# Performance work log

Measured on AMD Instinct MI355X. Metric: run time of the kernel, lower is better.

## Reference

```python
import jax, jax.numpy as jnp
import numpy as np

NUM_HEADS = 8
HEAD_DIM = 16  # d_model=128 / 8 heads
SCALE = HEAD_DIM ** -0.5


def setup_inputs() -> dict:
    key = jax.random.key(0)
    ks = jax.random.split(key, 12)
    B, A, K, L, D, M = 8, 64, 16, 30, 128, 128
    s = 1.0 / np.sqrt(D)
    inp = {
        "future_feat": jax.random.normal(ks[0], (B, A, L, D), jnp.float32),
        "geom_bias": jax.random.normal(ks[1], (B, A, K), jnp.float32),
        "Wq": jax.random.normal(ks[2], (D, M), jnp.float32) * s,
        "bq": jnp.zeros((M,), jnp.float32),
        "Wk": jax.random.normal(ks[3], (D, M), jnp.float32) * s,
        "bk": jnp.zeros((M,), jnp.float32),
        "Wv": jax.random.normal(ks[4], (D, M), jnp.float32) * s,
        "bv": jnp.zeros((M,), jnp.float32),
        "Wo": jax.random.normal(ks[5], (M, M), jnp.float32) * s,
        "bo": jnp.zeros((M,), jnp.float32),
        "neighbour_indices": jax.random.randint(ks[6], (B, A, K), 0, A),
        "neighbour_mask": jax.random.randint(ks[7], (B, A, K), 0, 2).astype(bool),
    }
    return inp


def reference(future_feat, geom_bias, Wq, bq, Wk, bk, Wv, bv, Wo, bo,
              neighbour_indices, neighbour_mask):
    B, A, L, D = future_feat.shape
    K = neighbour_indices.shape[2]
    H, HD = NUM_HEADS, HEAD_DIM

    # gather neighbour futures: [B, A, K, L, D]
    neighbours = jax.vmap(lambda f, idx: f[idx])(future_feat, neighbour_indices)

    q = (future_feat @ Wq + bq).reshape(B, A, L, H, HD).transpose(0, 1, 3, 2, 4)      # [B,A,H,Lq,hd]
    k = (neighbours @ Wk + bk).reshape(B, A, K, L, H, HD).transpose(0, 1, 4, 2, 3, 5)  # [B,A,H,K,Lk,hd]
    v = (neighbours @ Wv + bv).reshape(B, A, K, L, H, HD).transpose(0, 1, 4, 2, 3, 5)  # [B,A,H,K,Lk,hd]

    scores = jnp.einsum('bahqd,bahkld->bahqkl', q, k) * SCALE                          # [B,A,H,Lq,K,Lk]
    scores = scores + geom_bias[:, :, None, None, :, None]
    scores = jnp.where(neighbour_mask[:, :, None, None, :, None], scores, -jnp.inf)

    attn = jax.nn.softmax(scores.reshape(B, A, H, L, K * L), axis=-1)
    attn = jnp.nan_to_num(attn).reshape(B, A, H, L, K, L)

    ctx = jnp.einsum('bahqkl,bahkld->bahqd', attn, v)                                  # [B,A,H,Lq,hd]
    ctx = ctx.transpose(0, 1, 3, 2, 4).reshape(B, A, L, H * HD)
    out = ctx @ Wo + bo                                                                # [B,A,Lq,d_model]
    return out, attn
```

## Files before the change

kernel.cpp:

```cpp
#include <hip/hip_runtime.h>
#include <math.h>


#define NB 8
#define NA 64
#define NK 16
#define NL 30
#define ND 128
#define NM 128
#define NH 8
#define NHD 16
#define NKK (NK*NL)
#define FSCALE 0.25f
#define NROWS (NB*NA*NL)

typedef __attribute__((ext_vector_type(8))) short bf16x8;
typedef __attribute__((ext_vector_type(4))) float f32x4;

__device__ __forceinline__ unsigned short bf16r(float x) {
    unsigned u = __float_as_uint(x);
    return (unsigned short)((u + 0x7fffu + ((u >> 16) & 1u)) >> 16);
}

__global__ void detect_mask_fmt(const unsigned int* __restrict__ m, int* __restrict__ flag)
{
    __shared__ int not_i32, not_f32;
    if (threadIdx.x == 0) { not_i32 = 0; not_f32 = 0; }
    __syncthreads();
    for (int i = threadIdx.x; i < 2048; i += 256) {
        unsigned int u = m[i];
        if (u > 1u) not_i32 = 1;
        if (u != 0u && u != 0x3F800000u) not_f32 = 1;
    }
    __syncthreads();
    if (threadIdx.x == 0) *flag = (!not_i32) ? 0 : ((!not_f32) ? 1 : 2);
}

__global__ __launch_bounds__(256) void proj_qkv(
    const float* __restrict__ x,
    const float* __restrict__ Wq, const float* __restrict__ bq,
    const float* __restrict__ Wk, const float* __restrict__ bk,
    const float* __restrict__ Wv, const float* __restrict__ bv,
    float* __restrict__ qp, float* __restrict__ kp, float* __restrict__ vp)
{
    __shared__ __align__(16) float xs[NL][ND];
    const int ba = blockIdx.x;
    const float* xrow = x + (size_t)ba * NL * ND;
    for (int i = threadIdx.x; i < NL*ND/4; i += 256)
        ((float4*)xs)[i] = ((const float4*)xrow)[i];
    __syncthreads();

    const int j  = threadIdx.x & 127;
    const int rh = threadIdx.x >> 7;
    const float* Ws[3] = {Wq, Wk, Wv};
    const float* bs[3] = {bq, bk, bv};
    float*       Os[3] = {qp, kp, vp};

    #pragma unroll
    for (int m = 0; m < 3; ++m) {
        const float* W = Ws[m];
        float acc[15];
        #pragma unroll
        for (int r = 0; r < 15; ++r) acc[r] = 0.f;
        for (int d = 0; d < ND; d += 4) {
            float w0 = W[(d+0)*NM + j];
            float w1 = W[(d+1)*NM + j];
            float w2 = W[(d+2)*NM + j];
            float w3 = W[(d+3)*NM + j];
            #pragma unroll
            for (int r = 0; r < 15; ++r) {
                float4 xv = *(const float4*)&xs[rh*15 + r][d];
                acc[r] = fmaf(xv.x, w0, acc[r]);
                acc[r] = fmaf(xv.y, w1, acc[r]);
                acc[r] = fmaf(xv.z, w2, acc[r]);
                acc[r] = fmaf(xv.w, w3, acc[r]);
            }
        }
        float bj = bs[m][j];
        float* O = Os[m] + ((size_t)ba*NL + rh*15)*NM + j;
        #pragma unroll
        for (int r = 0; r < 15; ++r) O[r*NM] = acc[r] + bj;
    }
}

__global__ __launch_bounds__(128, 2) void attn_kernel(
    const float* __restrict__ qp, const float* __restrict__ kp, const float* __restrict__ vp,
    const float* __restrict__ geom_bias, const int* __restrict__ nidx,
    const void* __restrict__ nmask, const int* __restrict__ mask_fmt,
    float* __restrict__ attn_out, float* __restrict__ ctx_out)
{
    __shared__ __align__(16) short Kbf[NKK][16];
    __shared__ __align__(16) short Vt[16][488];
    __shared__ __align__(16) short pbuf[2][16][40];
    __shared__ float bias_ext[NKK];
    __shared__ float biasm[NK];
    __shared__ int   idx_s[NK];

    const int t    = threadIdx.x;
    const int blk  = blockIdx.x;
    const int h    = blk & 7;
    const int ba   = blk >> 3;
    const int b    = ba >> 6;
    const int lane = t & 63;
    const int w    = t >> 6;
    const int n    = lane & 15;
    const int quad = lane >> 4;

    if (t < NK) {
        idx_s[t] = nidx[ba*NK + t];
        const int fmt = *mask_fmt;
        bool mv;
        if (fmt == 0)      mv = ((const int*)nmask)[ba*NK + t] != 0;
        else if (fmt == 1) mv = ((const float*)nmask)[ba*NK + t] != 0.0f;
        else               mv = ((const unsigned char*)nmask)[ba*NK + t] != 0;
        biasm[t] = mv ? geom_bias[ba*NK + t] : -INFINITY;
    }
    __syncthreads();

    for (int i = t; i < NKK*4; i += 128) {
        const int kk = i >> 2, p = i & 3;
        const int kn = kk / NL, l = kk - kn*NL;
        const size_t off = ((size_t)(b*NA + idx_s[kn])*NL + l)*NM + h*NHD + p*4;
        float4 kv = *(const float4*)(kp + off);
        unsigned long long pk =
              (unsigned long long)bf16r(kv.x)
            | ((unsigned long long)bf16r(kv.y) << 16)
            | ((unsigned long long)bf16r(kv.z) << 32)
            | ((unsigned long long)bf16r(kv.w) << 48);
        *(unsigned long long*)&Kbf[kk][p*4] = pk;
        float4 vv = *(const float4*)(vp + off);
        Vt[p*4+0][kk] = (short)bf16r(vv.x);
        Vt[p*4+1][kk] = (short)bf16r(vv.y);
        Vt[p*4+2][kk] = (short)bf16r(vv.z);
        Vt[p*4+3][kk] = (short)bf16r(vv.w);
    }
    for (int i = t; i < NKK; i += 128) bias_ext[i] = biasm[i / NL];

    bf16x8 a_hi, a_lo;
    #pragma unroll
    for (int j = 0; j < 8; ++j) { a_hi[j] = 0; a_lo[j] = 0; }
    const int qrow = w*16 + n;
    if (quad < 2 && qrow < NL) {
        const float* qb = qp + ((size_t)ba*NL + qrow)*NM + h*NHD + quad*8;
        float4 x0 = *(const float4*)(qb);
        float4 x1 = *(const float4*)(qb + 4);
        float xv[8] = {x0.x,x0.y,x0.z,x0.w,x1.x,x1.y,x1.z,x1.w};
        #pragma unroll
        for (int j = 0; j < 8; ++j) {
            float x = xv[j] * FSCALE;
            unsigned short hb = bf16r(x);
            a_hi[j] = (short)hb;
            a_lo[j] = (short)bf16r(x - __uint_as_float(((unsigned)hb) << 16));
        }
    }
    __syncthreads();

    float s[NL][4];
    #pragma unroll
    for (int tt = 0; tt < NL; ++tt) {
        bf16x8 bfrag;
        #pragma unroll
        for (int j = 0; j < 8; ++j) bfrag[j] = 0;
        if (quad < 2)
            bfrag = *(const bf16x8*)&Kbf[tt*16 + n][quad*8];
        f32x4 acc = {0.f, 0.f, 0.f, 0.f};
        acc = __builtin_amdgcn_mfma_f32_16x16x32_bf16(a_hi, bfrag, acc, 0, 0, 0);
        acc = __builtin_amdgcn_mfma_f32_16x16x32_bf16(a_lo, bfrag, acc, 0, 0, 0);
        const float bv = bias_ext[tt*16 + n];
        s[tt][0] = acc[0] + bv;
        s[tt][1] = acc[1] + bv;
        s[tt][2] = acc[2] + bv;
        s[tt][3] = acc[3] + bv;
    }

    #pragma unroll
    for (int r = 0; r < 4; ++r) {
        float m = -INFINITY;
        #pragma unroll
        for (int tt = 0; tt < NL; ++tt) m = fmaxf(m, s[tt][r]);
        m = fmaxf(m, __shfl_xor(m, 1));
        m = fmaxf(m, __shfl_xor(m, 2));
        m = fmaxf(m, __shfl_xor(m, 4));
        m = fmaxf(m, __shfl_xor(m, 8));
        const bool ok = (m > -INFINITY);
        float sum = 0.f;
        #pragma unroll
        for (int tt = 0; tt < NL; ++tt) {
            float p = ok ? __expf(s[tt][r] - m) : 0.f;
            s[tt][r] = p;
            sum += p;
        }
        sum += __shfl_xor(sum, 1);
        sum += __shfl_xor(sum, 2);
        sum += __shfl_xor(sum, 4);
        sum += __shfl_xor(sum, 8);
        const float inv = (sum > 0.f) ? 1.f / sum : 0.f;
        #pragma unroll
        for (int tt = 0; tt < NL; ++tt) s[tt][r] *= inv;
    }

    const size_t abase = (size_t)blk * NL * NKK;
    #pragma unroll
    for (int r = 0; r < 4; ++r) {
        const int qr = w*16 + quad*4 + r;
        if (qr < NL) {
            float* ap = attn_out + abase + (size_t)qr * NKK + n;
            #pragma unroll
            for (int tt = 0; tt < NL; ++tt) ap[tt*16] = s[tt][r];
        }
    }

    f32x4 ctx = {0.f, 0.f, 0.f, 0.f};
    #pragma unroll
    for (int c = 0; c < 15; ++c) {
        #pragma unroll
        for (int r = 0; r < 4; ++r) {
            pbuf[w][quad*4 + r][n]      = (short)bf16r(s[2*c    ][r]);
            pbuf[w][quad*4 + r][16 + n] = (short)bf16r(s[2*c + 1][r]);
        }
        bf16x8 pa = *(const bf16x8*)&pbuf[w][n][quad*8];
        bf16x8 vb = *(const bf16x8*)&Vt[n][c*32 + quad*8];
        ctx = __builtin_amdgcn_mfma_f32_16x16x32_bf16(pa, vb, ctx, 0, 0, 0);
    }

    #pragma unroll
    for (int r = 0; r < 4; ++r) {
        const int qr = w*16 + quad*4 + r;
        if (qr < NL)
            ctx_out[((size_t)ba*NL + qr)*NM + h*NHD + n] = ctx[r];
    }
}

__global__ __launch_bounds__(256) void out_proj(
    const float* __restrict__ ctx, const float* __restrict__ Wo,
    const float* __restrict__ bo, float* __restrict__ out)
{
    __shared__ __align__(16) float xs[NL][ND];
    const int ba = blockIdx.x;
    const float* xrow = ctx + (size_t)ba * NL * ND;
    for (int i = threadIdx.x; i < NL*ND/4; i += 256)
        ((float4*)xs)[i] = ((const float4*)xrow)[i];
    __syncthreads();

    const int j  = threadIdx.x & 127;
    const int rh = threadIdx.x >> 7;
    float acc[15];
    #pragma unroll
    for (int r = 0; r < 15; ++r) acc[r] = 0.f;
    for (int d = 0; d < ND; d += 4) {
        float w0 = Wo[(d+0)*NM + j];
        float w1 = Wo[(d+1)*NM + j];
        float w2 = Wo[(d+2)*NM + j];
        float w3 = Wo[(d+3)*NM + j];
        #pragma unroll
        for (int r = 0; r < 15; ++r) {
            float4 xv = *(const float4*)&xs[rh*15 + r][d];
            acc[r] = fmaf(xv.x, w0, acc[r]);
            acc[r] = fmaf(xv.y, w1, acc[r]);
            acc[r] = fmaf(xv.z, w2, acc[r]);
            acc[r] = fmaf(xv.w, w3, acc[r]);
        }
    }
    float bj = bo[j];
    float* O = out + ((size_t)ba*NL + rh*15)*NM + j;
    #pragma unroll
    for (int r = 0; r < 15; ++r) O[r*NM] = acc[r] + bj;
}

extern "C" void kernel_launch(void* const* d_in, const int* in_sizes, int n_in,
                              void* d_out, int out_size, void* d_ws, size_t ws_size,
                              hipStream_t stream)
{
    const float* x    = (const float*)d_in[0];
    const float* gb   = (const float*)d_in[1];
    const float* Wq   = (const float*)d_in[2];
    const float* bq   = (const float*)d_in[3];
    const float* Wk   = (const float*)d_in[4];
    const float* bk   = (const float*)d_in[5];
    const float* Wv   = (const float*)d_in[6];
    const float* bv   = (const float*)d_in[7];
    const float* Wo   = (const float*)d_in[8];
    const float* bo   = (const float*)d_in[9];
    const int*   nidx = (const int*)d_in[10];
    const void*  nmask= d_in[11];

    float* out  = (float*)d_out;
    float* attn = out + (size_t)NROWS * NM;

    float* qp = (float*)d_ws;
    float* kp = qp + (size_t)NROWS * NM;
    float* vp = kp + (size_t)NROWS * NM;
    int* mflag = (int*)(vp + (size_t)NROWS * NM);

    detect_mask_fmt<<<1, 256, 0, stream>>>((const unsigned int*)nmask, mflag);
    proj_qkv<<<NB*NA, 256, 0, stream>>>(x, Wq, bq, Wk, bk, Wv, bv, qp, kp, vp);
    attn_kernel<<<NB*NA*NH, 128, 0, stream>>>(qp, kp, vp, gb, nidx, nmask, mflag,
                                              attn,  out);
    out_proj<<<NB*NA, 256, 0, stream>>>(out, Wo, bo, out);
}
```

Measured before the change: 389.6 us.

## Move Q/K/V and output projections to split-bf16 MFMA and coalesce attn stores

Replaces the scalar FP32 projection kernels with an MFMA kernel that uses hi/lo bf16 splits of activations and pre-transposed weights. A prep kernel converts the weights into this format and also folds in mask-format detection and bias staging. The attention kernel now stages probabilities in shared memory so that attn rows are written with contiguous float4 stores instead of strided scalar ones. The split-bf16 scheme (3 MFMAs) only approximates FP32 precision, and the extra shared-memory staging adds LDS traffic.

```diff
diff --git a/kernel.cpp b/kernel.cpp
--- a/kernel.cpp
+++ b/kernel.cpp
@@ -21,65 +21,122 @@
     unsigned u = __float_as_uint(x);
     return (unsigned short)((u + 0x7fffu + ((u >> 16) & 1u)) >> 16);
 }
-
-__global__ void detect_mask_fmt(const unsigned int* __restrict__ m, int* __restrict__ flag)
+__device__ __forceinline__ float bf16tof(unsigned short h) {
+    return __uint_as_float((unsigned)h << 16);
+}
+
+__global__ __launch_bounds__(256) void prep_kernel(
+    const float* __restrict__ Wq, const float* __restrict__ Wk,
+    const float* __restrict__ Wv, const float* __restrict__ Wo,
+    const float* __restrict__ bq, const float* __restrict__ bk,
+    const float* __restrict__ bv, const float* __restrict__ bo,
+    const unsigned int* __restrict__ nmask_u, int* __restrict__ mflag,
+    short* __restrict__ WtH, short* __restrict__ WtL, float* __restrict__ bias_ws)
 {
-    __shared__ int not_i32, not_f32;
-    if (threadIdx.x == 0) { not_i32 = 0; not_f32 = 0; }
+    const int t = threadIdx.x;
+    if (blockIdx.x == 8) {
+        __shared__ int not_i32, not_f32;
+        if (t == 0) { not_i32 = 0; not_f32 = 0; }
+        __syncthreads();
+        for (int i = t; i < 2048; i += 256) {
+            unsigned u = nmask_u[i];
+            if (u > 1u) not_i32 = 1;
+            if (u != 0u && u != 0x3F800000u) not_f32 = 1;
+        }
+        __syncthreads();
+        if (t == 0) *mflag = (!not_i32) ? 0 : ((!not_f32) ? 1 : 2);
+        if (t < 128) {
+            bias_ws[t]       = bq[t];
+            bias_ws[128 + t] = bk[t];
+            bias_ws[256 + t] = bv[t];
+            bias_ws[384 + t] = bo[t];
+        }
+        return;
+    }
+    const int m = blockIdx.x >> 1, half = blockIdx.x & 1, d0 = half * 64;
+    const float* W = (m == 0) ? Wq : (m == 1) ? Wk : (m == 2) ? Wv : Wo;
+    __shared__ __align__(16) float xs[64][132];
+    for (int i = t; i < 2048; i += 256) {
+        const int dd = i >> 5, j4 = (i & 31) * 4;
+        *(float4*)&xs[dd][j4] = *(const float4*)(W + (size_t)(d0 + dd) * NM + j4);
+    }
     __syncthreads();
-    for (int i = threadIdx.x; i < 2048; i += 256) {
-        unsigned int u = m[i];
-        if (u > 1u) not_i32 = 1;
-        if (u != 0u && u != 0x3F800000u) not_f32 = 1;
-    }
-    __syncthreads();
-    if (threadIdx.x == 0) *flag = (!not_i32) ? 0 : ((!not_f32) ? 1 : 2);
-}
-
-__global__ __launch_bounds__(256) void proj_qkv(
-    const float* __restrict__ x,
-    const float* __restrict__ Wq, const float* __restrict__ bq,
-    const float* __restrict__ Wk, const float* __restrict__ bk,
-    const float* __restrict__ Wv, const float* __restrict__ bv,
-    float* __restrict__ qp, float* __restrict__ kp, float* __restrict__ vp)
+    const int n = t >> 1, hs = t & 1;
+    unsigned short hb[32], lb[32];
+    #pragma unroll
+    for (int s = 0; s < 32; ++s) {
+        float v = xs[hs*32 + s][n];
+        unsigned short h = bf16r(v);
+        hb[s] = h;
+        lb[s] = bf16r(v - bf16tof(h));
+    }
+    const size_t base = (size_t)m * 16384 + (size_t)n * 128 + d0 + hs * 32;
+    #pragma unroll
+    for (int g = 0; g < 8; ++g) {
+        unsigned long long ph =
+              (unsigned long long)hb[4*g]
+            | ((unsigned long long)hb[4*g+1] << 16)
+            | ((unsigned long long)hb[4*g+2] << 32)
+            | ((unsigned long long)hb[4*g+3] << 48);
+        unsigned long long pl =
+              (unsigned long long)lb[4*g]
+            | ((unsigned long long)lb[4*g+1] << 16)
+            | ((unsigned long long)lb[4*g+2] << 32)
+            | ((unsigned long long)lb[4*g+3] << 48);
+        *(unsigned long long*)(WtH + base + g*4) = ph;
+        *(unsigned long long*)(WtL + base + g*4) = pl;
+    }
+}
+
+__global__ __launch_bounds__(256) void proj_mfma(
+    const float* X,
+    const short* __restrict__ WtH, const short* __restrict__ WtL,
+    const float* __restrict__ bias_ws,
+    float* Y, int mat_off)
 {
-    __shared__ __align__(16) float xs[NL][ND];
-    const int ba = blockIdx.x;
-    const float* xrow = x + (size_t)ba * NL * ND;
-    for (int i = threadIdx.x; i < NL*ND/4; i += 256)
-        ((float4*)xs)[i] = ((const float4*)xrow)[i];
-    __syncthreads();
-
-    const int j  = threadIdx.x & 127;
-    const int rh = threadIdx.x >> 7;
-    const float* Ws[3] = {Wq, Wk, Wv};
-    const float* bs[3] = {bq, bk, bv};
-    float*       Os[3] = {qp, kp, vp};
-
-    #pragma unroll
-    for (int m = 0; m < 3; ++m) {
-        const float* W = Ws[m];
-        float acc[15];
-        #pragma unroll
-        for (int r = 0; r < 15; ++r) acc[r] = 0.f;
-        for (int d = 0; d < ND; d += 4) {
-            float w0 = W[(d+0)*NM + j];
-            float w1 = W[(d+1)*NM + j];
-            float w2 = W[(d+2)*NM + j];
-            float w3 = W[(d+3)*NM + j];
-            #pragma unroll
-            for (int r = 0; r < 15; ++r) {
-                float4 xv = *(const float4*)&xs[rh*15 + r][d];
-                acc[r] = fmaf(xv.x, w0, acc[r]);
-                acc[r] = fmaf(xv.y, w1, acc[r]);
-                acc[r] = fmaf(xv.z, w2, acc[r]);
-                acc[r] = fmaf(xv.w, w3, acc[r]);
-            }
-        }
-        float bj = bs[m][j];
-        float* O = Os[m] + ((size_t)ba*NL + rh*15)*NM + j;
-        #pragma unroll
-        for (int r = 0; r < 15; ++r) O[r*NM] = acc[r] + bj;
+    const int m    = blockIdx.y;
+    const int mi   = mat_off + m;
+    const int rt   = blockIdx.x;
+    const int t    = threadIdx.x;
+    const int lane = t & 63, w = t >> 6;
+    const int n    = lane & 15, quad = lane >> 4;
+
+    const short* wh = WtH + (size_t)mi * 16384;
+    const short* wl = WtL + (size_t)mi * 16384;
+
+    const int arow = rt*64 + w*16 + n;
+    const float* xr = X + (size_t)arow * ND;
+    bf16x8 Ah[4], Al[4];
+    #pragma unroll
+    for (int ks = 0; ks < 4; ++ks) {
+        float4 x0 = *(const float4*)(xr + ks*32 + quad*8);
+        float4 x1 = *(const float4*)(xr + ks*32 + quad*8 + 4);
+        float xv[8] = {x0.x,x0.y,x0.z,x0.w,x1.x,x1.y,x1.z,x1.w};
+        #pragma unroll
+        for (int j = 0; j < 8; ++j) {
+            unsigned short h = bf16r(xv[j]);
+            Ah[ks][j] = (short)h;
+            Al[ks][j] = (short)bf16r(xv[j] - bf16tof(h));
+        }
+    }
+
+    float* ym = Y + (size_t)m * NROWS * NM;
+    #pragma unroll
+    for (int nt = 0; nt < 8; ++nt) {
+        f32x4 acc = {0.f, 0.f, 0.f, 0.f};
+        #pragma unroll
+        for (int ks = 0; ks < 4; ++ks) {
+            const size_t boff = (size_t)(nt*16 + n) * 128 + ks*32 + quad*8;
+            bf16x8 bh = *(const bf16x8*)(wh + boff);
+            bf16x8 bl = *(const bf16x8*)(wl + boff);
+            acc = __builtin_amdgcn_mfma_f32_16x16x32_bf16(Ah[ks], bh, acc, 0, 0, 0);
+            acc = __builtin_amdgcn_mfma_f32_16x16x32_bf16(Al[ks], bh, acc, 0, 0, 0);
+            acc = __builtin_amdgcn_mfma_f32_16x16x32_bf16(Ah[ks], bl, acc, 0, 0, 0);
+        }
+        const float bn = bias_ws[mi*128 + nt*16 + n];
+        #pragma unroll
+        for (int r = 0; r < 4; ++r)
+            ym[(size_t)(rt*64 + w*16 + quad*4 + r) * NM + nt*16 + n] = acc[r] + bn;
     }
 }
 
@@ -92,6 +149,7 @@
     __shared__ __align__(16) short Kbf[NKK][16];
     __shared__ __align__(16) short Vt[16][488];
     __shared__ __align__(16) short pbuf[2][16][40];
+    __shared__ __align__(16) float pf[2][16][34];
     __shared__ float bias_ext[NKK];
     __shared__ float biasm[NK];
     __shared__ int   idx_s[NK];
@@ -148,9 +206,9 @@
         #pragma unroll
         for (int j = 0; j < 8; ++j) {
             float x = xv[j] * FSCALE;
-            unsigned short hb = bf16r(x);
-            a_hi[j] = (short)hb;
-            a_lo[j] = (short)bf16r(x - __uint_as_float(((unsigned)hb) << 16));
+            unsigned short hbv = bf16r(x);
+            a_hi[j] = (short)hbv;
+            a_lo[j] = (short)bf16r(x - bf16tof(hbv));
         }
     }
     __syncthreads();
@@ -200,27 +258,33 @@
     }
 
     const size_t abase = (size_t)blk * NL * NKK;
-    #pragma unroll
-    for (int r = 0; r < 4; ++r) {
-        const int qr = w*16 + quad*4 + r;
-        if (qr < NL) {
-            float* ap = attn_out + abase + (size_t)qr * NKK + n;
-            #pragma unroll
-            for (int tt = 0; tt < NL; ++tt) ap[tt*16] = s[tt][r];
-        }
-    }
-
+    const int rr = lane >> 2, seg = lane & 3;
+    const int qr_st = w*16 + rr;
     f32x4 ctx = {0.f, 0.f, 0.f, 0.f};
     #pragma unroll
     for (int c = 0; c < 15; ++c) {
         #pragma unroll
         for (int r = 0; r < 4; ++r) {
-            pbuf[w][quad*4 + r][n]      = (short)bf16r(s[2*c    ][r]);
-            pbuf[w][quad*4 + r][16 + n] = (short)bf16r(s[2*c + 1][r]);
+            const float p0 = s[2*c][r], p1 = s[2*c + 1][r];
+            pbuf[w][quad*4 + r][n]      = (short)bf16r(p0);
+            pbuf[w][quad*4 + r][16 + n] = (short)bf16r(p1);
+            pf[w][quad*4 + r][n]        = p0;
+            pf[w][quad*4 + r][16 + n]   = p1;
         }
         bf16x8 pa = *(const bf16x8*)&pbuf[w][n][quad*8];
         bf16x8 vb = *(const bf16x8*)&Vt[n][c*32 + quad*8];
         ctx = __builtin_amdgcn_mfma_f32_16x16x32_bf16(pa, vb, ctx, 0, 0, 0);
+        if (qr_st < NL) {
+            float2 u0 = *(const float2*)&pf[w][rr][seg*8 + 0];
+            float2 u1 = *(const float2*)&pf[w][rr][seg*8 + 2];
+            float2 u2 = *(const float2*)&pf[w][rr][seg*8 + 4];
+            float2 u3 = *(const float2*)&pf[w][rr][seg*8 + 6];
+            float4 o0 = make_float4(u0.x, u0.y, u1.x, u1.y);
+            float4 o1 = make_float4(u2.x, u2.y, u3.x, u3.y);
+            float* ap = attn_out + abase + (size_t)qr_st*NKK + c*32 + seg*8;
+            *(float4*)ap       = o0;
+            *(float4*)(ap + 4) = o1;
+        }
     }
 
     #pragma unroll
@@ -229,42 +293,6 @@
         if (qr < NL)
             ctx_out[((size_t)ba*NL + qr)*NM + h*NHD + n] = ctx[r];
     }
-}
-
-__global__ __launch_bounds__(256) void out_proj(
-    const float* __restrict__ ctx, const float* __restrict__ Wo,
-    const float* __restrict__ bo, float* __restrict__ out)
-{
-    __shared__ __align__(16) float xs[NL][ND];
-    const int ba = blockIdx.x;
-    const float* xrow = ctx + (size_t)ba * NL * ND;
-    for (int i = threadIdx.x; i < NL*ND/4; i += 256)
-        ((float4*)xs)[i] = ((const float4*)xrow)[i];
-    __syncthreads();
-
-    const int j  = threadIdx.x & 127;
-    const int rh = threadIdx.x >> 7;
-    float acc[15];
-    #pragma unroll
-    for (int r = 0; r < 15; ++r) acc[r] = 0.f;
-    for (int d = 0; d < ND; d += 4) {
-        float w0 = Wo[(d+0)*NM + j];
-        float w1 = Wo[(d+1)*NM + j];
-        float w2 = Wo[(d+2)*NM + j];
-        float w3 = Wo[(d+3)*NM + j];
-        #pragma unroll
-        for (int r = 0; r < 15; ++r) {
-            float4 xv = *(const float4*)&xs[rh*15 + r][d];
-            acc[r] = fmaf(xv.x, w0, acc[r]);
-            acc[r] = fmaf(xv.y, w1, acc[r]);
-            acc[r] = fmaf(xv.z, w2, acc[r]);
-            acc[r] = fmaf(xv.w, w3, acc[r]);
-        }
-    }
-    float bj = bo[j];
-    float* O = out + ((size_t)ba*NL + rh*15)*NM + j;
-    #pragma unroll
-    for (int r = 0; r < 15; ++r) O[r*NM] = acc[r] + bj;
 }
 
 extern "C" void kernel_launch(void* const* d_in, const int* in_sizes, int n_in,
@@ -290,11 +318,18 @@
     float* qp = (float*)d_ws;
     float* kp = qp + (size_t)NROWS * NM;
     float* vp = kp + (size_t)NROWS * NM;
-    int* mflag = (int*)(vp + (size_t)NROWS * NM);
-
-    detect_mask_fmt<<<1, 256, 0, stream>>>((const unsigned int*)nmask, mflag);
-    proj_qkv<<<NB*NA, 256, 0, stream>>>(x, Wq, bq, Wk, bk, Wv, bv, qp, kp, vp);
+    int*   mflag   = (int*)(vp + (size_t)NROWS * NM);
+    float* bias_ws = (float*)(mflag + 4);
+    short* WtH     = (short*)(bias_ws + 512);
+    short* WtL     = WtH + 4 * 16384;
+
+    prep_kernel<<<9, 256, 0, stream>>>(Wq, Wk, Wv, Wo, bq, bk, bv, bo,
+                                       (const unsigned int*)nmask, mflag,
+                                       WtH, WtL, bias_ws);
+    dim3 gproj(NROWS/64, 3);
+    proj_mfma<<<gproj, 256, 0, stream>>>(x, WtH, WtL, bias_ws, qp, 0);
     attn_kernel<<<NB*NA*NH, 128, 0, stream>>>(qp, kp, vp, gb, nidx, nmask, mflag,
                                               attn,  out);
-    out_proj<<<NB*NA, 256, 0, stream>>>(out, Wo, bo, out);
-}
+    dim3 gout(NROWS/64, 1);
+    proj_mfma<<<gout, 256, 0, stream>>>(out, WtH, WtL, bias_ws, out, 3);
+}
```

After: 374.8 us. -3.8%, faster.
